# Optimization experiments

Measured on AMD Instinct MI355X. Metric: run time of the kernel, lower is better.

## Reference

```python
import jax, jax.numpy as jnp
import numpy as np

NUM_HEADS = 16


def setup_inputs() -> dict:
    key = jax.random.key(0)
    ks = jax.random.split(key, 11)
    B, S, D = 2, 8192, 1024
    scale = 1.0 / np.sqrt(D).astype(np.float32)
    return {
        "v": jax.random.normal(ks[0], (B, S, D), jnp.float32),
        "k": jax.random.normal(ks[1], (B, S, D), jnp.float32),
        "q": jax.random.normal(ks[2], (B, S, D), jnp.float32),
        "Wq": jax.random.normal(ks[3], (D, D), jnp.float32) * scale,
        "bq": jnp.zeros((D,), jnp.float32),
        "Wk": jax.random.normal(ks[4], (D, D), jnp.float32) * scale,
        "bk": jnp.zeros((D,), jnp.float32),
        "Wv": jax.random.normal(ks[5], (D, D), jnp.float32) * scale,
        "bv": jnp.zeros((D,), jnp.float32),
        "Wo": jax.random.normal(ks[6], (D, D), jnp.float32) * scale,
        "bo": jnp.zeros((D,), jnp.float32),
    }


def _mha(v, k, q, Wq, bq, Wk, bk, Wv, bv, Wo, bo):
    H = NUM_HEADS
    d_model = Wq.shape[1]
    depth = d_model // H
    # linear projections, split into heads: [B, S, H, depth]
    qh = (q @ Wq + bq).reshape(*q.shape[:-1], H, depth)
    kh = (k @ Wk + bk).reshape(*k.shape[:-1], H, depth)
    vh = (v @ Wv + bv).reshape(*v.shape[:-1], H, depth)
    # scaled dot-product attention. The original uses a chunked online-softmax
    # (memory-efficient attention, arXiv:2112.05682) which computes the exact
    # same softmax(QK^T/sqrt(d))V; we express it directly.
    scale = 1.0 / jnp.sqrt(jnp.asarray(depth, qh.dtype))
    logits = jnp.einsum('bqhd,bkhd->bhqk', qh * scale, kh,
                        precision=jax.lax.Precision.HIGHEST)
    attn = jax.nn.softmax(logits, axis=-1)
    out = jnp.einsum('bhqk,bkhd->bqhd', attn, vh,
                     precision=jax.lax.Precision.HIGHEST)
    out = out.reshape(*out.shape[:-2], d_model)
    return out @ Wo + bo


def reference(v, k, q, Wq, bq, Wk, bk, Wv, bv, Wo, bo):
    return _mha(v, k, q, Wq, bq, Wk, bk, Wv, bv, Wo, bo)
```

## Files before the change

kernel.cpp:

```cpp
#include <hip/hip_runtime.h>
#include <math.h>
#include <stdint.h>

#define H 16
#define Dm 1024
#define DH2 64
#define SLEN 8192
#define BATCH 2
#define KVBLK 64

#define WAIT_VM0 0x0F70

#if __has_builtin(__builtin_amdgcn_exp2f)
#define NEXP2(x) __builtin_amdgcn_exp2f(x)
#else
#define NEXP2(x) __builtin_exp2f(x)
#endif

typedef __attribute__((ext_vector_type(8))) short bf16x8;
typedef __attribute__((ext_vector_type(2))) float f32x2;
typedef __attribute__((ext_vector_type(4))) float f32x4;
typedef __attribute__((ext_vector_type(16))) float f32x16;
typedef __attribute__((ext_vector_type(4))) short short4v;
typedef __attribute__((ext_vector_type(4))) unsigned int uint4v;

#define MFMA16(a,b,c) __builtin_amdgcn_mfma_f32_16x16x32_bf16(a,b,c,0,0,0)
#define MFMA32(a,b,c) __builtin_amdgcn_mfma_f32_32x32x16_bf16(a,b,c,0,0,0)

static __device__ __forceinline__ short f2b(float f){
  unsigned u = __builtin_bit_cast(unsigned, f);
  u += 0x7fffu + ((u >> 16) & 1u);
  return (short)(u >> 16);
}

static __device__ __forceinline__ unsigned rne1(float f){
  unsigned u = __builtin_bit_cast(unsigned, f);
  return u + (0x7fffu + ((u >> 16) & 1u));
}
static __device__ __forceinline__ unsigned pack2(float lo, float hi){
  unsigned a = rne1(lo), b = rne1(hi);
  return __builtin_amdgcn_perm(b, a, 0x07060302u);
}

static __device__ __forceinline__ void gload16(const void* g, void* l){
  __builtin_amdgcn_global_load_lds((const __attribute__((address_space(1))) void*)g,
                                   (__attribute__((address_space(3))) void*)l, 16, 0, 0);
}

static __device__ __forceinline__ bf16x8 mkfrag(const f32x2* v, bool hib){
  unsigned p0 = pack2(v[0].x, v[0].y);
  unsigned p1 = pack2(v[1].x, v[1].y);
  unsigned p2 = pack2(v[2].x, v[2].y);
  unsigned p3 = pack2(v[3].x, v[3].y);
  unsigned s0 = (unsigned)__shfl_xor((int)p0, 32);
  unsigned s1 = (unsigned)__shfl_xor((int)p1, 32);
  unsigned s2 = (unsigned)__shfl_xor((int)p2, 32);
  unsigned s3 = (unsigned)__shfl_xor((int)p3, 32);
  uint4v u = hib ? (uint4v){s2, s3, p2, p3} : (uint4v){p0, p1, s0, s1};
  return __builtin_bit_cast(bf16x8, u);
}

struct S8 { f32x2 v[8]; };

__global__ __launch_bounds__(256) void transpose_w_kernel(
    const float* __restrict__ Wq, const float* __restrict__ Wk,
    const float* __restrict__ Wv, const float* __restrict__ Wo,
    short* __restrict__ WqT, short* __restrict__ WkT,
    short* __restrict__ WvT, short* __restrict__ WoT)
{
  const float* W; short* WT;
  switch (blockIdx.z){
    case 0: W = Wq; WT = WqT; break;
    case 1: W = Wk; WT = WkT; break;
    case 2: W = Wv; WT = WvT; break;
    default: W = Wo; WT = WoT; break;
  }
  __shared__ float t[32][33];
  int tx = threadIdx.x & 31, ty = threadIdx.x >> 5;
  int x0 = blockIdx.x * 32, y0 = blockIdx.y * 32;
  for (int j = 0; j < 4; ++j){
    int r = ty + j * 8;
    t[r][tx] = W[(size_t)(y0 + r) * Dm + x0 + tx];
  }
  __syncthreads();
  for (int j = 0; j < 4; ++j){
    int r = ty + j * 8;
    WT[(size_t)(x0 + r) * Dm + y0 + tx] = f2b(t[tx][r]);
  }
}

__global__ __launch_bounds__(256) void proj_kernel(
    const float* __restrict__ Aq, const float* __restrict__ Ak, const float* __restrict__ Av,
    const short* __restrict__ WqT, const short* __restrict__ WkT, const short* __restrict__ WvT,
    const float* __restrict__ bq, const float* __restrict__ bk, const float* __restrict__ bv,
    short* __restrict__ Qh, short* __restrict__ Kh, short* __restrict__ VhT)
{
  const float* A; const short* WT; const float* bias;
  int z = blockIdx.z;
  if (z == 0){ A = Aq; WT = WqT; bias = bq; }
  else if (z == 1){ A = Ak; WT = WkT; bias = bk; }
  else { A = Av; WT = WvT; bias = bv; }

  __shared__ __align__(16) char smem[34816];
  short (*As)[64] = (short(*)[64])smem;
  short* Bs = (short*)(smem + 16384);

  int tid = threadIdx.x;
  int lane = tid & 63, w = tid >> 6;
  int l15 = lane & 15, lh = lane >> 4;
  int wm = w >> 1, wn = w & 1;
  int m0 = blockIdx.x * 128, n0 = blockIdx.y * 128;

  f32x4 acc[4][4];
  for (int i = 0; i < 4; ++i)
    for (int j = 0; j < 4; ++j)
      acc[i][j] = (f32x4){0.f, 0.f, 0.f, 0.f};

  for (int ko = 0; ko < 16; ++ko){
    for (int j = 0; j < 8; ++j){
      int idx = j * 256 + tid;
      int r = idx >> 4, c4 = idx & 15;
      float4 a = *(const float4*)(A + (size_t)(m0 + r) * Dm + ko * 64 + c4 * 4);
      short4v p; p[0] = f2b(a.x); p[1] = f2b(a.y); p[2] = f2b(a.z); p[3] = f2b(a.w);
      *(short4v*)&As[r][c4 * 4] = p;
    }
    for (int j = 0; j < 4; ++j){
      int c = w * 4 + j;
      int row = c * 8 + (lane >> 3), seg = lane & 7;
      gload16(WT + (size_t)(n0 + row) * Dm + ko * 64 + seg * 8, Bs + c * 512);
    }
    __builtin_amdgcn_s_waitcnt(WAIT_VM0);
    __syncthreads();
    for (int kk = 0; kk < 2; ++kk){
      bf16x8 af[4];
      for (int i = 0; i < 4; ++i)
        af[i] = *(const bf16x8*)&As[wm * 64 + i * 16 + l15][kk * 32 + lh * 8];
      for (int jj = 0; jj < 4; ++jj){
        bf16x8 bfv = *(const bf16x8*)(Bs + (size_t)(wn * 64 + jj * 16 + l15) * 64 + kk * 32 + lh * 8);
        for (int i = 0; i < 4; ++i)
          acc[i][jj] = MFMA16(af[i], bfv, acc[i][jj]);
      }
    }
    __syncthreads();
  }

  if (z < 2){
    short* out = (z == 0) ? Qh : Kh;
    float scale = (z == 0) ? 0.18033688011112042f : 1.0f;
    for (int jj = 0; jj < 4; ++jj){
      int col = n0 + wn * 64 + jj * 16 + l15;
      float bb = bias[col];
      int h = col >> 6, d = col & 63;
      for (int i = 0; i < 4; ++i)
        for (int r = 0; r < 4; ++r){
          int row = m0 + wm * 64 + i * 16 + lh * 4 + r;
          int b = row >> 13, s = row & 8191;
          out[(((size_t)b * H + h) * SLEN + s) * DH2 + d] = f2b((acc[i][jj][r] + bb) * scale);
        }
    }
  } else {
    short (*Ct)[136] = (short(*)[136])smem;
    for (int jj = 0; jj < 4; ++jj){
      int colL = wn * 64 + jj * 16 + l15;
      float bb = bias[n0 + colL];
      for (int i = 0; i < 4; ++i)
        for (int r = 0; r < 4; ++r){
          int rowL = wm * 64 + i * 16 + lh * 4 + r;
          Ct[colL][rowL] = f2b(acc[i][jj][r] + bb);
        }
    }
    __syncthreads();
    int b = m0 >> 13, s0 = m0 & 8191;
    for (int p = 0; p < 8; ++p){
      int rowC = p * 16 + (tid >> 4), seg = tid & 15;
      int4 vv = *(const int4*)&Ct[rowC][seg * 8];
      int ngl = n0 + rowC, h = ngl >> 6, d = ngl & 63;
      *(int4*)&VhT[(((size_t)b * H + h) * DH2 + d) * SLEN + s0 + seg * 8] = vv;
    }
  }
}

__global__ __launch_bounds__(512, 2) void attn_kernel(
    const short* __restrict__ Qh, const short* __restrict__ Kh,
    const short* __restrict__ VhT, short* __restrict__ attn_out)
{
  __shared__ __align__(16) short Ktile[2][4096];
  __shared__ __align__(16) short Vtile[2][4096];
  __shared__ float redbuf[8][32];

  const int tid = threadIdx.x;
  const int lane = tid & 63;
  const int w = tid >> 6;
  const int l31 = lane & 31;
  const int hi = lane >> 5;
  const bool hib = (hi != 0);
  const int bh = blockIdx.y;
  const int q0 = blockIdx.x * 256 + w * 32;

  const short* Qbase = Qh + ((size_t)bh * SLEN + q0) * DH2;
  const short* Kbase = Kh + (size_t)bh * SLEN * DH2;
  const short* Vbase = VhT + (size_t)bh * DH2 * SLEN;

  bf16x8 qf[4];
#pragma unroll
  for (int ds = 0; ds < 4; ++ds)
    qf[ds] = *(const bf16x8*)(Qbase + (size_t)l31 * DH2 + ds * 16 + hi * 8);

  f32x16 Oa0, Oa1;
#pragma unroll
  for (int i = 0; i < 16; ++i){ Oa0[i] = 0.f; Oa1[i] = 0.f; }
  float l_run = 0.f;

  int koff[4];
#pragma unroll
  for (int ds = 0; ds < 4; ++ds)
    koff[ds] = l31 * 64 + (((ds * 2 + hi) ^ (l31 & 7)) * 8);
  int voff[2][4];
#pragma unroll
  for (int n = 0; n < 2; ++n)
#pragma unroll
    for (int st = 0; st < 4; ++st)
      voff[n][st] = (n * 32 + l31) * 64 + (((st * 2 + hi) ^ (l31 & 7)) * 8);

  const short* spK = Kbase + (size_t)(tid >> 3) * DH2 + (((tid & 7) ^ ((tid >> 3) & 7)) * 8);
  const short* spV = Vbase + (size_t)(tid >> 3) * SLEN + (((tid & 7) ^ ((tid >> 3) & 7)) * 8);
  short* dK0 = Ktile[0] + tid * 8; short* dK1 = Ktile[1] + tid * 8;
  short* dV0 = Vtile[0] + tid * 8; short* dV1 = Vtile[1] + tid * 8;

  gload16(spK, dK0); gload16(spV, dV0);
  spK += (size_t)KVBLK * DH2; spV += KVBLK;

  const int NT = SLEN / KVBLK;

  auto tile = [&](const short* Kt, const short* Vt, bool do_stage,
                  short* dK, short* dV){
    __builtin_amdgcn_s_waitcnt(WAIT_VM0);
    __syncthreads();
    if (do_stage){
      gload16(spK, dK);
      gload16(spV, dV);
      spK += (size_t)KVBLK * DH2; spV += KVBLK;
    }

    f32x16 sa0, sa1;
#pragma unroll
    for (int i = 0; i < 16; ++i){ sa0[i] = 0.f; sa1[i] = 0.f; }
#pragma unroll
    for (int ds = 0; ds < 4; ++ds){
      bf16x8 kf0 = *(const bf16x8*)(Kt + koff[ds]);
      bf16x8 kf1 = *(const bf16x8*)(Kt + koff[ds] + 32 * 64);
      sa0 = MFMA32(kf0, qf[ds], sa0);
      sa1 = MFMA32(kf1, qf[ds], sa1);
    }

    S8 t0 = __builtin_bit_cast(S8, sa0);
    S8 t1 = __builtin_bit_cast(S8, sa1);
#pragma unroll
    for (int i = 0; i < 8; ++i){
      t0.v[i].x = NEXP2(t0.v[i].x);
      t0.v[i].y = NEXP2(t0.v[i].y);
      t1.v[i].x = NEXP2(t1.v[i].x);
      t1.v[i].y = NEXP2(t1.v[i].y);
    }

    f32x2 s0 = ((t0.v[0] + t0.v[1]) + (t0.v[2] + t0.v[3])) +
               ((t0.v[4] + t0.v[5]) + (t0.v[6] + t0.v[7]));
    f32x2 s1 = ((t1.v[0] + t1.v[1]) + (t1.v[2] + t1.v[3])) +
               ((t1.v[4] + t1.v[5]) + (t1.v[6] + t1.v[7]));
    f32x2 st = s0 + s1;
    l_run += st.x + st.y;

    bf16x8 pa0 = mkfrag(&t0.v[0], hib);
    bf16x8 pa1 = mkfrag(&t0.v[4], hib);
    bf16x8 pa2 = mkfrag(&t1.v[0], hib);
    bf16x8 pa3 = mkfrag(&t1.v[4], hib);

    bf16x8 vb;
    vb = *(const bf16x8*)(Vt + voff[0][0]); Oa0 = MFMA32(pa0, vb, Oa0);
    vb = *(const bf16x8*)(Vt + voff[1][0]); Oa1 = MFMA32(pa0, vb, Oa1);
    vb = *(const bf16x8*)(Vt + voff[0][1]); Oa0 = MFMA32(pa1, vb, Oa0);
    vb = *(const bf16x8*)(Vt + voff[1][1]); Oa1 = MFMA32(pa1, vb, Oa1);
    vb = *(const bf16x8*)(Vt + voff[0][2]); Oa0 = MFMA32(pa2, vb, Oa0);
    vb = *(const bf16x8*)(Vt + voff[1][2]); Oa1 = MFMA32(pa2, vb, Oa1);
    vb = *(const bf16x8*)(Vt + voff[0][3]); Oa0 = MFMA32(pa3, vb, Oa0);
    vb = *(const bf16x8*)(Vt + voff[1][3]); Oa1 = MFMA32(pa3, vb, Oa1);
  };

  for (int kt = 0; kt < NT; kt += 2){
    tile(Ktile[0], Vtile[0], true,          dK1, dV1);
    tile(Ktile[1], Vtile[1], kt + 2 < NT,   dK0, dV0);
  }

  float l_tot = l_run + __shfl_xor(l_run, 32);
  float inv = 1.0f / l_tot;
  redbuf[w][l31] = inv;
  int b = bh >> 4, h = bh & 15;
#pragma unroll
  for (int j = 0; j < 4; ++j){
    f32x4 iv = *(const f32x4*)&redbuf[w][j * 8 + hi * 4];
#pragma unroll
    for (int i = 0; i < 4; ++i){
      int qi = j * 8 + hi * 4 + i;
      size_t rowoff = ((size_t)b * SLEN + q0 + qi) * Dm + h * 64;
      attn_out[rowoff + l31]      = f2b(Oa0[j * 4 + i] * iv[i]);
      attn_out[rowoff + 32 + l31] = f2b(Oa1[j * 4 + i] * iv[i]);
    }
  }
}

__global__ __launch_bounds__(256) void oproj_kernel(
    const short* __restrict__ Aattn, const short* __restrict__ WoT,
    const float* __restrict__ bo, float* __restrict__ out)
{
  __shared__ __align__(16) char smem[32768];
  short* As = (short*)smem;
  short* Bs = (short*)(smem + 16384);

  int tid = threadIdx.x;
  int lane = tid & 63, w = tid >> 6;
  int l15 = lane & 15, lh = lane >> 4;
  int wm = w >> 1, wn = w & 1;
  int m0 = blockIdx.x * 128, n0 = blockIdx.y * 128;

  f32x4 acc[4][4];
  for (int i = 0; i < 4; ++i)
    for (int j = 0; j < 4; ++j)
      acc[i][j] = (f32x4){0.f, 0.f, 0.f, 0.f};

  for (int ko = 0; ko < 16; ++ko){
    for (int j = 0; j < 4; ++j){
      int c = w * 4 + j;
      int row = c * 8 + (lane >> 3), seg = lane & 7;
      gload16(Aattn + (size_t)(m0 + row) * Dm + ko * 64 + seg * 8, As + c * 512);
      gload16(WoT   + (size_t)(n0 + row) * Dm + ko * 64 + seg * 8, Bs + c * 512);
    }
    __builtin_amdgcn_s_waitcnt(WAIT_VM0);
    __syncthreads();
    for (int kk = 0; kk < 2; ++kk){
      bf16x8 af[4];
      for (int i = 0; i < 4; ++i)
        af[i] = *(const bf16x8*)(As + (size_t)(wm * 64 + i * 16 + l15) * 64 + kk * 32 + lh * 8);
      for (int jj = 0; jj < 4; ++jj){
        bf16x8 bfv = *(const bf16x8*)(Bs + (size_t)(wn * 64 + jj * 16 + l15) * 64 + kk * 32 + lh * 8);
        for (int i = 0; i < 4; ++i)
          acc[i][jj] = MFMA16(af[i], bfv, acc[i][jj]);
      }
    }
    __syncthreads();
  }
  for (int jj = 0; jj < 4; ++jj){
    int col = n0 + wn * 64 + jj * 16 + l15;
    float bb = bo[col];
    for (int i = 0; i < 4; ++i)
      for (int r = 0; r < 4; ++r){
        int row = m0 + wm * 64 + i * 16 + lh * 4 + r;
        out[(size_t)row * Dm + col] = acc[i][jj][r] + bb;
      }
  }
}

extern "C" void kernel_launch(void* const* d_in, const int* in_sizes, int n_in,
                              void* d_out, int out_size, void* d_ws, size_t ws_size,
                              hipStream_t stream)
{
  const float* v  = (const float*)d_in[0];
  const float* k  = (const float*)d_in[1];
  const float* q  = (const float*)d_in[2];
  const float* Wq = (const float*)d_in[3];
  const float* bq = (const float*)d_in[4];
  const float* Wk = (const float*)d_in[5];
  const float* bk = (const float*)d_in[6];
  const float* Wv = (const float*)d_in[7];
  const float* bv = (const float*)d_in[8];
  const float* Wo = (const float*)d_in[9];
  const float* bo = (const float*)d_in[10];
  float* out = (float*)d_out;

  char* ws = (char*)d_ws;
  const size_t MB = 1u << 20;
  short* WqT = (short*)(ws + 0 * MB);
  short* WkT = (short*)(ws + 2 * MB);
  short* WvT = (short*)(ws + 4 * MB);
  short* WoT = (short*)(ws + 6 * MB);
  short* Qh  = (short*)(ws + 8 * MB);
  short* Kh  = (short*)(ws + 40 * MB);
  short* VhT = (short*)(ws + 72 * MB);
  short* Ao  = (short*)(ws + 104 * MB);

  transpose_w_kernel<<<dim3(32, 32, 4), 256, 0, stream>>>(Wq, Wk, Wv, Wo, WqT, WkT, WvT, WoT);
  proj_kernel<<<dim3(128, 8, 3), 256, 0, stream>>>(q, k, v, WqT, WkT, WvT, bq, bk, bv, Qh, Kh, VhT);
  attn_kernel<<<dim3(32, 32), 512, 0, stream>>>(Qh, Kh, VhT, Ao);
  oproj_kernel<<<dim3(128, 8), 256, 0, stream>>>(Ao, WoT, bo, out);
}
```

Before: 1.013 ms.

## Permute V^T storage so P fragments pack with cvt_pk without cross-lane shuffles

Replaces the manual round-to-nearest bf16 packing plus four cross-half-wave shuffles per P fragment with hardware v_cvt_pk_bf16_f32 instructions. To keep the MFMA operand pairing correct without the shuffles, the V projection epilogue now writes V^T with a permuted key order inside each 16-element group. This removes permute and shuffle work from the attention inner loop, at the cost of narrower 8-byte scattered stores in the projection epilogue. It depends on the permuted key order matching the MFMA fragment layout exactly.

```diff
diff --git a/kernel.cpp b/kernel.cpp
--- a/kernel.cpp
+++ b/kernel.cpp
@@ -23,6 +23,7 @@
 typedef __attribute__((ext_vector_type(16))) float f32x16;
 typedef __attribute__((ext_vector_type(4))) short short4v;
 typedef __attribute__((ext_vector_type(4))) unsigned int uint4v;
+typedef __attribute__((ext_vector_type(2))) int int2v;
 
 #define MFMA16(a,b,c) __builtin_amdgcn_mfma_f32_16x16x32_bf16(a,b,c,0,0,0)
 #define MFMA32(a,b,c) __builtin_amdgcn_mfma_f32_32x32x16_bf16(a,b,c,0,0,0)
@@ -33,30 +34,18 @@
   return (short)(u >> 16);
 }
 
-static __device__ __forceinline__ unsigned rne1(float f){
-  unsigned u = __builtin_bit_cast(unsigned, f);
-  return u + (0x7fffu + ((u >> 16) & 1u));
-}
-static __device__ __forceinline__ unsigned pack2(float lo, float hi){
-  unsigned a = rne1(lo), b = rne1(hi);
-  return __builtin_amdgcn_perm(b, a, 0x07060302u);
-}
-
 static __device__ __forceinline__ void gload16(const void* g, void* l){
   __builtin_amdgcn_global_load_lds((const __attribute__((address_space(1))) void*)g,
                                    (__attribute__((address_space(3))) void*)l, 16, 0, 0);
 }
 
-static __device__ __forceinline__ bf16x8 mkfrag(const f32x2* v, bool hib){
-  unsigned p0 = pack2(v[0].x, v[0].y);
-  unsigned p1 = pack2(v[1].x, v[1].y);
-  unsigned p2 = pack2(v[2].x, v[2].y);
-  unsigned p3 = pack2(v[3].x, v[3].y);
-  unsigned s0 = (unsigned)__shfl_xor((int)p0, 32);
-  unsigned s1 = (unsigned)__shfl_xor((int)p1, 32);
-  unsigned s2 = (unsigned)__shfl_xor((int)p2, 32);
-  unsigned s3 = (unsigned)__shfl_xor((int)p3, 32);
-  uint4v u = hib ? (uint4v){s2, s3, p2, p3} : (uint4v){p0, p1, s0, s1};
+static __device__ __forceinline__ bf16x8 mkfrag_pk(const f32x2* v){
+  unsigned p0, p1, p2, p3;
+  asm("v_cvt_pk_bf16_f32 %0, %1, %2" : "=v"(p0) : "v"(v[0].x), "v"(v[0].y));
+  asm("v_cvt_pk_bf16_f32 %0, %1, %2" : "=v"(p1) : "v"(v[1].x), "v"(v[1].y));
+  asm("v_cvt_pk_bf16_f32 %0, %1, %2" : "=v"(p2) : "v"(v[2].x), "v"(v[2].y));
+  asm("v_cvt_pk_bf16_f32 %0, %1, %2" : "=v"(p3) : "v"(v[3].x), "v"(v[3].y));
+  uint4v u = (uint4v){p0, p1, p2, p3};
   return __builtin_bit_cast(bf16x8, u);
 }
 
@@ -175,7 +164,14 @@
       int rowC = p * 16 + (tid >> 4), seg = tid & 15;
       int4 vv = *(const int4*)&Ct[rowC][seg * 8];
       int ngl = n0 + rowC, h = ngl >> 6, d = ngl & 63;
-      *(int4*)&VhT[(((size_t)b * H + h) * DH2 + d) * SLEN + s0 + seg * 8] = vv;
+      size_t base = (((size_t)b * H + h) * DH2 + d) * SLEN + s0;
+      int sA = seg * 8;
+      int b16 = sA & ~15;
+      int half = (sA >> 3) & 1;
+      int2v lo = (int2v){ ((int*)&vv)[0], ((int*)&vv)[1] };
+      int2v hi2 = (int2v){ ((int*)&vv)[2], ((int*)&vv)[3] };
+      *(int2v*)&VhT[base + b16 + half * 4]     = lo;
+      *(int2v*)&VhT[base + b16 + 8 + half * 4] = hi2;
     }
   }
 }
@@ -193,7 +189,6 @@
   const int w = tid >> 6;
   const int l31 = lane & 31;
   const int hi = lane >> 5;
-  const bool hib = (hi != 0);
   const int bh = blockIdx.y;
   const int q0 = blockIdx.x * 256 + w * 32;
 
@@ -270,10 +265,10 @@
     f32x2 st = s0 + s1;
     l_run += st.x + st.y;
 
-    bf16x8 pa0 = mkfrag(&t0.v[0], hib);
-    bf16x8 pa1 = mkfrag(&t0.v[4], hib);
-    bf16x8 pa2 = mkfrag(&t1.v[0], hib);
-    bf16x8 pa3 = mkfrag(&t1.v[4], hib);
+    bf16x8 pa0 = mkfrag_pk(&t0.v[0]);
+    bf16x8 pa1 = mkfrag_pk(&t0.v[4]);
+    bf16x8 pa2 = mkfrag_pk(&t1.v[0]);
+    bf16x8 pa3 = mkfrag_pk(&t1.v[4]);
 
     bf16x8 vb;
     vb = *(const bf16x8*)(Vt + voff[0][0]); Oa0 = MFMA32(pa0, vb, Oa0);
```

New measurement: 829.3 us. -18.1%, faster.
